# Kernel tuning notes

Measured on AMD Instinct MI355X. Metric: run time of the kernel, lower is better.

Reference implementation:

```python
import jax, jax.numpy as jnp
import numpy as np

N = 100000   # nodes
E = 1200000  # directed edges
F_IN, HID, EMB = 5, 64, 16

def setup_inputs() -> dict:
    key = jax.random.key(0)
    ks = jax.random.split(key, 12)
    # node features: [lambda, mu, is_comp, is_AND, is_OR]
    lam = jax.random.uniform(ks[0], (N, 1), jnp.float32) * 0.01
    mu = jax.random.uniform(ks[1], (N, 1), jnp.float32) * 0.1
    node_type = jax.random.randint(ks[2], (N,), 0, 3)
    onehot = jax.nn.one_hot(node_type, 3, dtype=jnp.float32)
    x = jnp.concatenate([lam, mu, onehot], axis=1)  # [N,5]
    edge_index = jax.random.randint(ks[3], (2, E), 0, N, dtype=jnp.int32)

    def lin(k, fi, fo):
        s = 1.0 / np.sqrt(fi)
        return jax.random.uniform(k, (fi, fo), jnp.float32, -s, s)

    return {
        "x": x, "edge_index": edge_index,
        "T": jnp.float32(100.0), "T_max": jnp.float32(500.0),
        "W1": lin(ks[4], F_IN, HID), "b1": jnp.zeros((HID,), jnp.float32),
        "W2": lin(ks[5], HID, HID), "b2": jnp.zeros((HID,), jnp.float32),
        "W3": lin(ks[6], HID, EMB), "b3": jnp.zeros((EMB,), jnp.float32),
        "P1": lin(ks[7], EMB + 8, 64), "pb1": jnp.zeros((64,), jnp.float32),
        "P2": lin(ks[8], 64, 32), "pb2": jnp.zeros((32,), jnp.float32),
        "P3": lin(ks[9], 32, 4), "pb3": jnp.zeros((4,), jnp.float32),
    }

def gcn_conv(h_in, src, dst, W, b):
    """PyG GCNConv: add self-loops, symmetric D^-1/2 (A+I) D^-1/2 norm."""
    h = h_in @ W  # [N,F]
    # degree with self-loops: 1 + in-degree (count on target nodes)
    deg = jax.ops.segment_sum(jnp.ones((E,), jnp.float32), dst, num_segments=N) + 1.0
    dinv = jax.lax.rsqrt(deg)  # [N]
    norm = dinv[src] * dinv[dst]  # [E]
    agg = jax.ops.segment_sum(h[src] * norm[:, None], dst, num_segments=N)
    agg = agg + h * (dinv * dinv)[:, None]  # self-loop term norm = 1/deg
    return agg + b

def reference(x, edge_index, T, T_max, W1, b1, W2, b2, W3, b3,
              P1, pb1, P2, pb2, P3, pb3):
    src, dst = edge_index[0], edge_index[1]
    h = jax.nn.relu(gcn_conv(x, src, dst, W1, b1))
    h = jax.nn.relu(gcn_conv(h, src, dst, W2, b2))
    h = gcn_conv(h, src, dst, W3, b3)
    embedding = jnp.mean(h, axis=0, keepdims=True)  # global_mean_pool, batch=0 -> [1,EMB]

    T_norm = T / T_max
    comp = x[:, 2]
    n_comp = jnp.sum(comp)
    n_AND = jnp.sum(x[:, 3])
    n_OR = jnp.sum(x[:, 4])
    safe = jnp.maximum(n_comp, 1.0)
    has = n_comp > 0
    avg_lambda = jnp.where(has, jnp.sum(x[:, 0] * comp) / safe, 0.0)
    avg_mu = jnp.where(has, jnp.sum(x[:, 1] * comp) / safe, 0.0)
    t_inv = 1.0 / (1.0 + T_norm)
    gf = jnp.stack([n_comp, n_AND, n_OR, n_AND + n_OR,
                    avg_lambda, avg_mu, T_norm * 50.0, t_inv * 50.0])[None, :]  # [1,8]

    emb = jnp.concatenate([embedding, gf], axis=1)  # [1,24]
    hmlp = jax.nn.relu(emb @ P1 + pb1)
    hmlp = jax.nn.relu(hmlp @ P2 + pb2)
    raw = hmlp @ P3 + pb3  # [1,4]

    val = jax.nn.softplus(raw + 2.0)
    alpha_min = 1.0 + val[:, 0]
    alpha_max = alpha_min + val[:, 1] + 0.5
    beta_min = 1.0 + val[:, 2]
    beta_max = beta_min + val[:, 3] + 0.5
    out = jnp.stack([alpha_min, alpha_max, beta_min, beta_max], axis=1)  # [1,4]
    return out, emb
```

## Files before the change

kernel.cpp:

```cpp
#include <hip/hip_runtime.h>

#define NN 100000
#define NE 1200000
#define NB_SCAN ((NN + 255) / 256)
#define NPASS 8
#define WNODES ((NN + NPASS - 1) / NPASS)
#define EB 128

__global__ void k_hist(const int* __restrict__ ei, int* __restrict__ cnt) {
    int i = blockIdx.x * 256 + threadIdx.x;
    if (i < NE) atomicAdd(&cnt[ei[NE + i]], 1);
}

__global__ void k_scan_block(const int* __restrict__ cnt, int* __restrict__ incl,
                             int* __restrict__ bsum, float* __restrict__ dinv) {
    __shared__ int s[256];
    int t = threadIdx.x;
    int i = blockIdx.x * 256 + t;
    int v = (i < NN) ? cnt[i] : 0;
    if (i < NN) dinv[i] = rsqrtf((float)v + 1.0f);
    s[t] = v;
    __syncthreads();
    for (int off = 1; off < 256; off <<= 1) {
        int add = (t >= off) ? s[t - off] : 0;
        __syncthreads();
        s[t] += add;
        __syncthreads();
    }
    if (i < NN) incl[i] = s[t];
    if (t == 255) bsum[blockIdx.x] = s[255];
}

__global__ void k_scan_bsum(int* __restrict__ bsum) {
    __shared__ int s[512];
    int t = threadIdx.x;
    s[t] = (t < NB_SCAN) ? bsum[t] : 0;
    __syncthreads();
    for (int off = 1; off < 512; off <<= 1) {
        int add = (t >= off) ? s[t - off] : 0;
        __syncthreads();
        s[t] += add;
        __syncthreads();
    }
    if (t < NB_SCAN) bsum[t] = s[t];
}

__global__ void k_scan_add(const int* __restrict__ cnt, const int* __restrict__ incl,
                           const int* __restrict__ bsum, int* __restrict__ rowptr) {
    int i = blockIdx.x * 256 + threadIdx.x;
    if (i >= NN) return;
    int base = (blockIdx.x > 0) ? bsum[blockIdx.x - 1] : 0;
    rowptr[i] = base + incl[i] - cnt[i];
    if (i == 0) rowptr[NN] = NE;
}

__global__ void k_scatter_win(const int* __restrict__ ei, const int* __restrict__ rowptr,
                              int* __restrict__ cursor, int* __restrict__ srcs) {
    int pass = blockIdx.x / EB;
    int blk  = blockIdx.x % EB;
    int lo = pass * WNODES;
    int hi = lo + WNODES;
    for (int e = blk * 256 + threadIdx.x; e < NE; e += EB * 256) {
        int dst = ei[NE + e];
        if (dst >= lo && dst < hi) {
            int pos = rowptr[dst] + atomicAdd(&cursor[dst], 1);
            srcs[pos] = ei[e];
        }
    }
}

__global__ void k_aggx(const int* __restrict__ rowptr, const int* __restrict__ srcs,
                       const float* __restrict__ dinv, const float* __restrict__ x,
                       float* __restrict__ aggx) {
    int t = threadIdx.x;
    int n = blockIdx.x * 4 + (t >> 6);
    if (n >= NN) return;
    int lane = t & 63, c = lane & 7, slot = lane >> 3;
    int e0 = rowptr[n], e1 = rowptr[n + 1];
    float es = 0.f;
    if (c < 5) {
        for (int j = e0 + slot; j < e1; j += 8) {
            int s = srcs[j];
            es += x[(size_t)s * 5 + c] * dinv[s];
        }
    }
    es += __shfl_xor(es, 8, 64);
    es += __shfl_xor(es, 16, 64);
    es += __shfl_xor(es, 32, 64);
    float dvn = dinv[n];
    if (slot == 0 && c < 5)
        aggx[(size_t)n * 5 + c] = es * dvn + x[(size_t)n * 5 + c] * dvn * dvn;
}

__global__ void k_lin_first(const float* __restrict__ aggx, const float* __restrict__ W,
                            const float* __restrict__ b, float* __restrict__ h) {
    __shared__ float Ws[5 * 64];
    __shared__ float bs[64];
    int t = threadIdx.x;
    for (int i = t; i < 320; i += 256) Ws[i] = W[i];
    if (t < 64) bs[t] = b[t];
    __syncthreads();
    int r = t >> 6, c = t & 63;
    int row = blockIdx.x * 4 + r;
    if (row >= NN) return;
    float acc = bs[c];
#pragma unroll
    for (int k = 0; k < 5; k++) acc += aggx[(size_t)row * 5 + k] * Ws[k * 64 + c];
    h[(size_t)row * 64 + c] = fmaxf(acc, 0.f);
}

__global__ void k_lin64(const float* __restrict__ in, const float* __restrict__ W,
                        float* __restrict__ h) {
    __shared__ float Ws[64 * 64];
    __shared__ float rows[256];
    int t = threadIdx.x;
    for (int i = t; i < 4096; i += 256) Ws[i] = W[i];
    int base = blockIdx.x * 4;
    int gidx = base * 64 + t;
    rows[t] = (gidx < NN * 64) ? in[gidx] : 0.f;
    __syncthreads();
    int r = t >> 6, c = t & 63, row = base + r;
    if (row >= NN) return;
    float acc = 0.f;
#pragma unroll
    for (int k = 0; k < 64; k++) acc += rows[r * 64 + k] * Ws[k * 64 + c];
    h[(size_t)row * 64 + c] = acc;
}

__global__ void k_lin3(const float* __restrict__ in, const float* __restrict__ W,
                       float* __restrict__ h) {
    __shared__ float Ws[64 * 16];
    __shared__ float rows[16 * 64];
    int t = threadIdx.x;
    for (int i = t; i < 1024; i += 256) Ws[i] = W[i];
    int base = blockIdx.x * 16;
    for (int i = t; i < 1024; i += 256) {
        int g = base * 64 + i;
        rows[i] = (g < NN * 64) ? in[g] : 0.f;
    }
    __syncthreads();
    int r = t >> 4, c = t & 15, row = base + r;
    if (row >= NN) return;
    float acc = 0.f;
#pragma unroll
    for (int k = 0; k < 64; k++) acc += rows[r * 64 + k] * Ws[k * 16 + c];
    h[(size_t)row * 16 + c] = acc;
}

template <bool RELU>
__global__ void k_agg64(const int* __restrict__ rowptr, const int* __restrict__ srcs,
                        const float* __restrict__ dinv, const float* __restrict__ h,
                        const float* __restrict__ b, float* __restrict__ out) {
    int t = threadIdx.x;
    int n = blockIdx.x * 4 + (t >> 6);
    if (n >= NN) return;
    int c = t & 63;
    int e0 = rowptr[n], e1 = rowptr[n + 1];
    float dvn = dinv[n];
    float acc0 = 0.f, acc1 = 0.f, acc2 = 0.f, acc3 = 0.f;
    int j = e0;
    for (; j + 3 < e1; j += 4) {
        int s0 = srcs[j], s1 = srcs[j + 1], s2 = srcs[j + 2], s3 = srcs[j + 3];
        float w0 = dinv[s0], w1 = dinv[s1], w2 = dinv[s2], w3 = dinv[s3];
        acc0 += h[(size_t)s0 * 64 + c] * w0;
        acc1 += h[(size_t)s1 * 64 + c] * w1;
        acc2 += h[(size_t)s2 * 64 + c] * w2;
        acc3 += h[(size_t)s3 * 64 + c] * w3;
    }
    for (; j < e1; j++) {
        int s0 = srcs[j];
        acc0 += h[(size_t)s0 * 64 + c] * dinv[s0];
    }
    float v = ((acc0 + acc1) + (acc2 + acc3)) * dvn
            + h[(size_t)n * 64 + c] * dvn * dvn + b[c];
    if (RELU) v = fmaxf(v, 0.f);
    out[(size_t)n * 64 + c] = v;
}

__global__ void k_agg16_reduce(const int* __restrict__ rowptr, const int* __restrict__ srcs,
                               const float* __restrict__ dinv, const float* __restrict__ h,
                               const float* __restrict__ b, float* __restrict__ red) {
    int t = threadIdx.x;
    int lane = t & 63, wv = t >> 6;
    int c = lane & 15, slot = lane >> 4;
    int gw = blockIdx.x * 4 + wv;
    int nw = gridDim.x * 4;
    float acc = 0.f;
    for (int n = gw; n < NN; n += nw) {
        int e0 = rowptr[n], e1 = rowptr[n + 1];
        float dvn = dinv[n];
        float es = 0.f;
        for (int j = e0 + slot; j < e1; j += 4) {
            int s0 = srcs[j];
            es += h[(size_t)s0 * 16 + c] * dinv[s0];
        }
        es += __shfl_xor(es, 16, 64);
        es += __shfl_xor(es, 32, 64);
        if (slot == 0)
            acc += es * dvn + h[(size_t)n * 16 + c] * dvn * dvn + b[c];
    }
    __shared__ float s[4][16];
    if (slot == 0) s[wv][c] = acc;
    __syncthreads();
    if (t < 16) atomicAdd(&red[t], (s[0][t] + s[1][t]) + (s[2][t] + s[3][t]));
}

__global__ void k_reduce_gf(const float* __restrict__ x, float* __restrict__ red) {
    int t = threadIdx.x;
    float sc = 0, sa = 0, so = 0, sl = 0, sm = 0;
    for (int i = blockIdx.x * 256 + t; i < NN; i += gridDim.x * 256) {
        float lam = x[i * 5 + 0], mu = x[i * 5 + 1];
        float c = x[i * 5 + 2], a = x[i * 5 + 3], o = x[i * 5 + 4];
        sc += c; sa += a; so += o; sl += lam * c; sm += mu * c;
    }
    __shared__ float s[256];
    float vals[5] = {sc, sa, so, sl, sm};
#pragma unroll
    for (int k = 0; k < 5; k++) {
        s[t] = vals[k];
        __syncthreads();
        for (int off = 128; off > 0; off >>= 1) {
            if (t < off) s[t] += s[t + off];
            __syncthreads();
        }
        if (t == 0) atomicAdd(&red[16 + k], s[0]);
        __syncthreads();
    }
}

__device__ __forceinline__ float softplus_f(float x) {
    return (x > 20.f) ? x : log1pf(expf(x));
}

__global__ void k_mlp(const float* __restrict__ red,
                      const float* __restrict__ T, const float* __restrict__ Tmax,
                      const float* __restrict__ P1, const float* __restrict__ pb1,
                      const float* __restrict__ P2, const float* __restrict__ pb2,
                      const float* __restrict__ P3, const float* __restrict__ pb3,
                      float* __restrict__ out) {
    __shared__ float emb[24];
    __shared__ float hm1[64];
    __shared__ float hm2[32];
    __shared__ float val[4];
    int t = threadIdx.x;
    if (t < 16) emb[t] = red[t] / (float)NN;
    if (t == 0) {
        float sc = red[16], sa = red[17], so = red[18], sl = red[19], sm = red[20];
        float Tn = T[0] / Tmax[0];
        emb[16] = sc;
        emb[17] = sa;
        emb[18] = so;
        emb[19] = sa + so;
        float safe = fmaxf(sc, 1.0f);
        bool has = sc > 0.f;
        emb[20] = has ? sl / safe : 0.f;
        emb[21] = has ? sm / safe : 0.f;
        emb[22] = Tn * 50.f;
        emb[23] = (1.f / (1.f + Tn)) * 50.f;
    }
    __syncthreads();
    {
        float acc = pb1[t];
#pragma unroll
        for (int k = 0; k < 24; k++) acc += emb[k] * P1[k * 64 + t];
        hm1[t] = fmaxf(acc, 0.f);
    }
    __syncthreads();
    if (t < 32) {
        float acc = pb2[t];
#pragma unroll
        for (int k = 0; k < 64; k++) acc += hm1[k] * P2[k * 32 + t];
        hm2[t] = fmaxf(acc, 0.f);
    }
    __syncthreads();
    if (t < 4) {
        float acc = pb3[t];
#pragma unroll
        for (int k = 0; k < 32; k++) acc += hm2[k] * P3[k * 4 + t];
        val[t] = softplus_f(acc + 2.0f);
    }
    __syncthreads();
    if (t == 0) {
        float amin = 1.f + val[0];
        float amax = amin + val[1] + 0.5f;
        float bmin = 1.f + val[2];
        float bmax = bmin + val[3] + 0.5f;
        out[0] = amin; out[1] = amax; out[2] = bmin; out[3] = bmax;
    }
    if (t >= 4 && t < 28) out[t] = emb[t - 4];
}

extern "C" void kernel_launch(void* const* d_in, const int* in_sizes, int n_in,
                              void* d_out, int out_size, void* d_ws, size_t ws_size,
                              hipStream_t stream) {
    const float* x    = (const float*)d_in[0];
    const int*   ei   = (const int*)d_in[1];
    const float* T    = (const float*)d_in[2];
    const float* Tmax = (const float*)d_in[3];
    const float* W1   = (const float*)d_in[4];
    const float* b1   = (const float*)d_in[5];
    const float* W2   = (const float*)d_in[6];
    const float* b2   = (const float*)d_in[7];
    const float* W3   = (const float*)d_in[8];
    const float* b3   = (const float*)d_in[9];
    const float* P1   = (const float*)d_in[10];
    const float* pb1  = (const float*)d_in[11];
    const float* P2   = (const float*)d_in[12];
    const float* pb2  = (const float*)d_in[13];
    const float* P3   = (const float*)d_in[14];
    const float* pb3  = (const float*)d_in[15];
    float* out = (float*)d_out;

    char* w = (char*)d_ws;
    float* bufH   = (float*)w;                 w += (size_t)NN * 64 * 4;
    float* bufA   = (float*)w;                 w += (size_t)NN * 64 * 4;
    int*   cnt    = (int*)w;                   w += (size_t)NN * 4;
    int*   cursor = (int*)w;                   w += (size_t)NN * 4;
    float* red    = (float*)w;                 w += 32 * 4;
    float* dinv   = (float*)w;                 w += (size_t)NN * 4;
    int*   incl   = (int*)w;                   w += (size_t)NN * 4;
    int*   rowptr = (int*)w;                   w += (size_t)(NN + 1) * 4;
    int*   srcs   = (int*)w;                   w += (size_t)NE * 4;
    int*   bsum   = (int*)w;                   w += 512 * 4;
    float* aggx   = (float*)w;                 w += (size_t)NN * 5 * 4;

    hipMemsetAsync(cnt, 0, (2 * (size_t)NN + 32) * sizeof(int), stream);

    k_hist<<<(NE + 255) / 256, 256, 0, stream>>>(ei, cnt);
    k_scan_block<<<NB_SCAN, 256, 0, stream>>>(cnt, incl, bsum, dinv);
    k_scan_bsum<<<1, 512, 0, stream>>>(bsum);
    k_scan_add<<<NB_SCAN, 256, 0, stream>>>(cnt, incl, bsum, rowptr);
    k_scatter_win<<<NPASS * EB, 256, 0, stream>>>(ei, rowptr, cursor, srcs);

    k_aggx<<<(NN + 3) / 4, 256, 0, stream>>>(rowptr, srcs, dinv, x, aggx);
    k_lin_first<<<(NN + 3) / 4, 256, 0, stream>>>(aggx, W1, b1, bufA);

    k_lin64<<<(NN + 3) / 4, 256, 0, stream>>>(bufA, W2, bufH);
    k_agg64<true><<<(NN + 3) / 4, 256, 0, stream>>>(rowptr, srcs, dinv, bufH, b2, bufA);

    k_lin3<<<(NN + 15) / 16, 256, 0, stream>>>(bufA, W3, bufH);
    k_agg16_reduce<<<2048, 256, 0, stream>>>(rowptr, srcs, dinv, bufH, b3, red);

    k_reduce_gf<<<1024, 256, 0, stream>>>(x, red);
    k_mlp<<<1, 64, 0, stream>>>(red, T, Tmax, P1, pb1, P2, pb2, P3, pb3, out);
}
```

Before: 506.5 us.

## Replace float atomics with per-block partials and interleave scatter passes

The final 16-wide and global-feature reductions now write per-block partial sums, which the MLP kernel (now 256 threads) reduces instead of relying on float atomicAdd. This makes the result deterministic and removes the need to memset the red buffer. Block counts drop (2048->1024 for agg16, 1024->64 for gf). The scatter kernel also interleaves pass and block indices so all node windows run at the same time rather than one after another, which may change atomic contention and cache behaviour.

```diff
diff --git a/kernel.cpp b/kernel.cpp
--- a/kernel.cpp
+++ b/kernel.cpp
@@ -6,6 +6,8 @@
 #define NPASS 8
 #define WNODES ((NN + NPASS - 1) / NPASS)
 #define EB 128
+#define GF_BLOCKS 64
+#define P16_BLOCKS 1024
 
 __global__ void k_hist(const int* __restrict__ ei, int* __restrict__ cnt) {
     int i = blockIdx.x * 256 + threadIdx.x;
@@ -56,8 +58,8 @@
 
 __global__ void k_scatter_win(const int* __restrict__ ei, const int* __restrict__ rowptr,
                               int* __restrict__ cursor, int* __restrict__ srcs) {
-    int pass = blockIdx.x / EB;
-    int blk  = blockIdx.x % EB;
+    int pass = blockIdx.x & (NPASS - 1);
+    int blk  = blockIdx.x / NPASS;
     int lo = pass * WNODES;
     int hi = lo + WNODES;
     for (int e = blk * 256 + threadIdx.x; e < NE; e += EB * 256) {
@@ -177,9 +179,9 @@
     out[(size_t)n * 64 + c] = v;
 }
 
-__global__ void k_agg16_reduce(const int* __restrict__ rowptr, const int* __restrict__ srcs,
-                               const float* __restrict__ dinv, const float* __restrict__ h,
-                               const float* __restrict__ b, float* __restrict__ red) {
+__global__ void k_agg16_part(const int* __restrict__ rowptr, const int* __restrict__ srcs,
+                             const float* __restrict__ dinv, const float* __restrict__ h,
+                             const float* __restrict__ b, float* __restrict__ part16) {
     int t = threadIdx.x;
     int lane = t & 63, wv = t >> 6;
     int c = lane & 15, slot = lane >> 4;
@@ -202,10 +204,10 @@
     __shared__ float s[4][16];
     if (slot == 0) s[wv][c] = acc;
     __syncthreads();
-    if (t < 16) atomicAdd(&red[t], (s[0][t] + s[1][t]) + (s[2][t] + s[3][t]));
-}
-
-__global__ void k_reduce_gf(const float* __restrict__ x, float* __restrict__ red) {
+    if (t < 16) part16[blockIdx.x * 16 + t] = (s[0][t] + s[1][t]) + (s[2][t] + s[3][t]);
+}
+
+__global__ void k_gf_part(const float* __restrict__ x, float* __restrict__ gfpart) {
     int t = threadIdx.x;
     float sc = 0, sa = 0, so = 0, sl = 0, sm = 0;
     for (int i = blockIdx.x * 256 + t; i < NN; i += gridDim.x * 256) {
@@ -223,7 +225,7 @@
             if (t < off) s[t] += s[t + off];
             __syncthreads();
         }
-        if (t == 0) atomicAdd(&red[16 + k], s[0]);
+        if (t == 0) gfpart[blockIdx.x * 5 + k] = s[0];
         __syncthreads();
     }
 }
@@ -232,20 +234,38 @@
     return (x > 20.f) ? x : log1pf(expf(x));
 }
 
-__global__ void k_mlp(const float* __restrict__ red,
+__global__ void k_mlp(const float* __restrict__ part16, const float* __restrict__ gfpart,
                       const float* __restrict__ T, const float* __restrict__ Tmax,
                       const float* __restrict__ P1, const float* __restrict__ pb1,
                       const float* __restrict__ P2, const float* __restrict__ pb2,
                       const float* __restrict__ P3, const float* __restrict__ pb3,
                       float* __restrict__ out) {
+    __shared__ float s[256];
     __shared__ float emb[24];
     __shared__ float hm1[64];
     __shared__ float hm2[32];
     __shared__ float val[4];
     int t = threadIdx.x;
-    if (t < 16) emb[t] = red[t] / (float)NN;
+    {
+        int c = t & 15, g = t >> 4;
+        float acc = 0.f;
+        for (int r = g; r < P16_BLOCKS; r += 16) acc += part16[r * 16 + c];
+        s[t] = acc;
+        __syncthreads();
+        for (int off = 128; off >= 16; off >>= 1) {
+            if (t < off) s[t] += s[t + off];
+            __syncthreads();
+        }
+        if (t < 16) emb[t] = s[t] / (float)NN;
+    }
+    if (t < 5) {
+        float acc = 0.f;
+        for (int r = 0; r < GF_BLOCKS; r++) acc += gfpart[r * 5 + t];
+        s[t] = acc;
+    }
+    __syncthreads();
     if (t == 0) {
-        float sc = red[16], sa = red[17], so = red[18], sl = red[19], sm = red[20];
+        float sc = s[0], sa = s[1], so = s[2], sl = s[3], sm = s[4];
         float Tn = T[0] / Tmax[0];
         emb[16] = sc;
         emb[17] = sa;
@@ -259,7 +279,7 @@
         emb[23] = (1.f / (1.f + Tn)) * 50.f;
     }
     __syncthreads();
-    {
+    if (t < 64) {
         float acc = pb1[t];
 #pragma unroll
         for (int k = 0; k < 24; k++) acc += emb[k] * P1[k * 64 + t];
@@ -316,15 +336,16 @@
     float* bufA   = (float*)w;                 w += (size_t)NN * 64 * 4;
     int*   cnt    = (int*)w;                   w += (size_t)NN * 4;
     int*   cursor = (int*)w;                   w += (size_t)NN * 4;
-    float* red    = (float*)w;                 w += 32 * 4;
     float* dinv   = (float*)w;                 w += (size_t)NN * 4;
     int*   incl   = (int*)w;                   w += (size_t)NN * 4;
     int*   rowptr = (int*)w;                   w += (size_t)(NN + 1) * 4;
     int*   srcs   = (int*)w;                   w += (size_t)NE * 4;
     int*   bsum   = (int*)w;                   w += 512 * 4;
     float* aggx   = (float*)w;                 w += (size_t)NN * 5 * 4;
-
-    hipMemsetAsync(cnt, 0, (2 * (size_t)NN + 32) * sizeof(int), stream);
+    float* part16 = (float*)w;                 w += (size_t)P16_BLOCKS * 16 * 4;
+    float* gfpart = (float*)w;                 w += (size_t)GF_BLOCKS * 5 * 4;
+
+    hipMemsetAsync(cnt, 0, 2 * (size_t)NN * sizeof(int), stream);
 
     k_hist<<<(NE + 255) / 256, 256, 0, stream>>>(ei, cnt);
     k_scan_block<<<NB_SCAN, 256, 0, stream>>>(cnt, incl, bsum, dinv);
@@ -339,8 +360,8 @@
     k_agg64<true><<<(NN + 3) / 4, 256, 0, stream>>>(rowptr, srcs, dinv, bufH, b2, bufA);
 
     k_lin3<<<(NN + 15) / 16, 256, 0, stream>>>(bufA, W3, bufH);
-    k_agg16_reduce<<<2048, 256, 0, stream>>>(rowptr, srcs, dinv, bufH, b3, red);
-
-    k_reduce_gf<<<1024, 256, 0, stream>>>(x, red);
-    k_mlp<<<1, 64, 0, stream>>>(red, T, Tmax, P1, pb1, P2, pb2, P3, pb3, out);
-}
+    k_agg16_part<<<P16_BLOCKS, 256, 0, stream>>>(rowptr, srcs, dinv, bufH, b3, part16);
+
+    k_gf_part<<<GF_BLOCKS, 256, 0, stream>>>(x, gfpart);
+    k_mlp<<<1, 256, 0, stream>>>(part16, gfpart, T, Tmax, P1, pb1, P2, pb2, P3, pb3, out);
+}
```

Result: faster. 470.4 us (-7.1%).
